# Optimization experiments

Hardware: AMD Instinct MI355X
Metric: run time of the kernel (lower is better)

## Reference

```python
import jax, jax.numpy as jnp
import numpy as np

EPS = 1e-06


def setup_inputs() -> dict:
    key = jax.random.key(0)
    ks = jax.random.split(key, 6)
    B, L, N = 64, 4096, 128
    F = L // 2 + 1  # 2049 rfft bins
    E = 8
    x = jax.random.normal(ks[0], (B, L, N), dtype=jnp.float32)
    band_boundaries = jax.random.normal(ks[1], (E - 1,), dtype=jnp.float32)
    # gate: Linear(F,F) -> ReLU -> Linear(F,E); stored as [in,out] matrices
    gate_w1 = jax.random.normal(ks[2], (F, F), dtype=jnp.float32) * (1.0 / np.sqrt(F))
    gate_b1 = jnp.zeros((F,), dtype=jnp.float32)
    gate_w2 = jax.random.normal(ks[3], (F, E), dtype=jnp.float32) * (1.0 / np.sqrt(F))
    gate_b2 = jnp.zeros((E,), dtype=jnp.float32)
    return {"x": x, "band_boundaries": band_boundaries,
            "gate_w1": gate_w1, "gate_b1": gate_b1,
            "gate_w2": gate_w2, "gate_b2": gate_b2}


def reference(x, band_boundaries, gate_w1, gate_b1, gate_w2, gate_b2):
    # FrequencyMoE forward (residual_add=True). x: [B, L, N]
    B, L, N = x.shape
    F = L // 2 + 1
    xN = jnp.transpose(x, (0, 2, 1))  # [B, N, L]
    mean = jnp.mean(xN, axis=-1, keepdims=True)
    var = jnp.var(xN, axis=-1, keepdims=True) + EPS
    # NOTE: original code computes x_norm then overwrites with xN (normalization skipped),
    # but still rescales the reconstruction by sqrt(var) and adds mean back. Faithful copy.
    freq = jnp.fft.rfft(xN, n=L, axis=-1)  # [B, N, F] complex64

    # learnable band boundaries -> integer bin indices (non-differentiable, as in torch .long())
    bb = jnp.sort(jax.nn.sigmoid(band_boundaries))
    b01 = jnp.concatenate([jnp.zeros((1,), bb.dtype), bb, jnp.ones((1,), bb.dtype)])
    idx = jnp.clip((b01 * F).astype(jnp.int32), 0, F)
    idx = idx.at[-1].set(F)  # [E+1]

    bins = jnp.arange(F)
    # per-expert frequency masks [E, F]: bin in [idx[e], idx[e+1])
    masks = ((bins[None, :] >= idx[:-1, None]) & (bins[None, :] < idx[1:, None])).astype(xN.dtype)

    # gating on mean magnitude spectrum over variables
    mag = jnp.mean(jnp.abs(freq), axis=1)  # [B, F]
    h = jax.nn.relu(mag @ gate_w1 + gate_b1)
    weights = jax.nn.softmax(h @ gate_w2 + gate_b2, axis=-1)  # [B, E]

    # fused weighted-mask combination: sum_e w[b,e]*mask[e,f] applied to spectrum
    wmask = weights @ masks  # [B, F]
    freq_out = freq * wmask[:, None, :]
    x_rec = jnp.fft.irfft(freq_out, n=L, axis=-1)  # [B, N, L]
    x_rec = x_rec * jnp.sqrt(var) + mean
    outN = xN + x_rec  # residual_add=True
    return jnp.transpose(outN, (0, 2, 1))  # [B, L, N]
```

## Files before the change

kernel.cpp:

```cpp
#include <hip/hip_runtime.h>

#define B_ 64
#define L_ 4096
#define N_ 128
#define F_ 2049
#define M_ 2048

__device__ __forceinline__ int pidx(int a) { return a + (a >> 3); }

__device__ __forceinline__ float2 cadd(float2 a, float2 b) { return make_float2(a.x + b.x, a.y + b.y); }
__device__ __forceinline__ float2 csub(float2 a, float2 b) { return make_float2(a.x - b.x, a.y - b.y); }
__device__ __forceinline__ float2 cmul(float2 a, float2 b) {
  return make_float2(a.x * b.x - a.y * b.y, a.x * b.y + a.y * b.x);
}
template <int SGN>
__device__ __forceinline__ float2 mulsi(float2 a) {
  return (SGN > 0) ? make_float2(-a.y, a.x) : make_float2(a.y, -a.x);
}

template <int SGN>
__device__ __forceinline__ void dft8(float2* v) {
  const float C = 0.70710678118654752f;
  float2 t0 = cadd(v[0], v[4]), t1 = csub(v[0], v[4]);
  float2 t2 = cadd(v[2], v[6]), t3 = mulsi<SGN>(csub(v[2], v[6]));
  float2 t4 = cadd(v[1], v[5]), t5 = csub(v[1], v[5]);
  float2 t6 = cadd(v[3], v[7]), t7 = mulsi<SGN>(csub(v[3], v[7]));
  float2 u0 = cadd(t0, t2), u1 = csub(t0, t2);
  float2 u2 = cadd(t1, t3), u3 = csub(t1, t3);
  float2 u4 = cadd(t4, t6), u5 = csub(t4, t6);
  float2 u6 = cadd(t5, t7), u7 = csub(t5, t7);
  float2 w1 = make_float2(C, (SGN > 0) ? C : -C);
  float2 w3 = make_float2(-C, (SGN > 0) ? C : -C);
  float2 a5 = mulsi<SGN>(u5);
  float2 b6 = cmul(u6, w1);
  float2 b7 = cmul(u7, w3);
  v[0] = cadd(u0, u4); v[4] = csub(u0, u4);
  v[2] = cadd(u1, a5); v[6] = csub(u1, a5);
  v[1] = cadd(u2, b6); v[5] = csub(u2, b6);
  v[3] = cadd(u3, b7); v[7] = csub(u3, b7);
}

template <int SGN>
__device__ __forceinline__ void dft4(float2* v) {
  float2 e0 = cadd(v[0], v[2]), e1 = csub(v[0], v[2]);
  float2 o0 = cadd(v[1], v[3]), o1 = mulsi<SGN>(csub(v[1], v[3]));
  v[0] = cadd(e0, o0); v[2] = csub(e0, o0);
  v[1] = cadd(e1, o1); v[3] = csub(e1, o1);
}

template <int SGN>
__device__ __forceinline__ void tw8(float2* v, int pm) {
  float ang = (float)pm * 0.00306796157577128245f;
  float sv, cv;
  __sincosf(ang, &sv, &cv);
  float2 w = make_float2(cv, (SGN > 0) ? sv : -sv);
  float2 wk = w;
  v[1] = cmul(v[1], wk);
#pragma unroll
  for (int k = 2; k < 8; ++k) { wk = cmul(wk, w); v[k] = cmul(v[k], wk); }
}

template <int SGN>
__device__ __forceinline__ void fft2048(float2* __restrict__ buf, float2* v, int t) {
  dft8<SGN>(v);
  tw8<SGN>(v, t);
  __syncthreads();
#pragma unroll
  for (int k = 0; k < 8; ++k) buf[pidx(8 * t + k)] = v[k];
  __syncthreads();
#pragma unroll
  for (int r = 0; r < 8; ++r) v[r] = buf[pidx(t + 256 * r)];
  dft8<SGN>(v);
  tw8<SGN>(v, t & ~7);
  __syncthreads();
  {
    int q = t & 7, p = t >> 3;
#pragma unroll
    for (int k = 0; k < 8; ++k) buf[pidx(q + 8 * (8 * p + k))] = v[k];
  }
  __syncthreads();
#pragma unroll
  for (int r = 0; r < 8; ++r) v[r] = buf[pidx(t + 256 * r)];
  dft8<SGN>(v);
  tw8<SGN>(v, t & ~63);
  __syncthreads();
  {
    int q = t & 63, p = t >> 6;
#pragma unroll
    for (int k = 0; k < 8; ++k) buf[pidx(q + 64 * (8 * p + k))] = v[k];
  }
  __syncthreads();
  float2 w0[4], w1s[4];
#pragma unroll
  for (int r = 0; r < 4; ++r) {
    w0[r] = buf[pidx(t + 512 * r)];
    w1s[r] = buf[pidx(t + 256 + 512 * r)];
  }
  dft4<SGN>(w0);
  dft4<SGN>(w1s);
  __syncthreads();
#pragma unroll
  for (int k = 0; k < 4; ++k) {
    buf[pidx(t + 512 * k)] = w0[k];
    buf[pidx(t + 256 + 512 * k)] = w1s[k];
  }
  __syncthreads();
}

__global__ __launch_bounds__(256) void transpose_k(const float* __restrict__ in,
                                                   float* __restrict__ out,
                                                   int R, int C) {
  __shared__ float tile[32][33];
  const float* ip = in + (size_t)blockIdx.z * R * C;
  float* op = out + (size_t)blockIdx.z * R * C;
  int c0 = blockIdx.x * 32;
  int r0 = blockIdx.y * 32;
  int x = threadIdx.x;
  int y = threadIdx.y;
#pragma unroll
  for (int i = 0; i < 4; ++i)
    tile[y + 8 * i][x] = ip[(size_t)(r0 + y + 8 * i) * C + (c0 + x)];
  __syncthreads();
#pragma unroll
  for (int i = 0; i < 4; ++i)
    op[(size_t)(c0 + y + 8 * i) * R + (r0 + x)] = tile[x][y + 8 * i];
}

template <int S>
__global__ __launch_bounds__(256) void p1_fft_mag(const float* __restrict__ src,
                                                  float* __restrict__ magsum) {
  __shared__ float2 buf[2304];
  int t = threadIdx.x;
  int blk = blockIdx.x;
  int b = blk >> 7;
  int n = blk & 127;
  const float* base = (S == 1) ? (src + (size_t)blk * L_)
                               : (src + (size_t)b * L_ * N_ + n);
  float2 v[8];
  if (S == 1) {
    const float2* r2 = (const float2*)base;
#pragma unroll
    for (int r = 0; r < 8; ++r) v[r] = r2[t + 256 * r];
  } else {
#pragma unroll
    for (int r = 0; r < 8; ++r) {
      int k = t + 256 * r;
      v[r] = make_float2(base[(size_t)(2 * k) * S], base[(size_t)(2 * k + 1) * S]);
    }
  }
  fft2048<-1>(buf, v, t);

  float* msum = magsum + (size_t)b * F_;
#pragma unroll
  for (int i = 0; i < 8; ++i) {
    int f = t + 256 * i;
    float mg;
    if (f == 0) {
      float2 z = buf[pidx(0)];
      mg = fabsf(z.x + z.y);
      atomicAdd(&msum[2048], fabsf(z.x - z.y));
    } else {
      float2 zf = buf[pidx(f)], zm = buf[pidx(2048 - f)];
      float Are = 0.5f * (zf.x + zm.x), Aim = 0.5f * (zf.y - zm.y);
      float Bre = 0.5f * (zf.y + zm.y), Bim = -0.5f * (zf.x - zm.x);
      float ang = (float)f * 0.00153398078788564117f;
      float sv, cv;
      __sincosf(ang, &sv, &cv);
      float Xre = Are + cv * Bre + sv * Bim;
      float Xim = Aim + cv * Bim - sv * Bre;
      mg = sqrtf(Xre * Xre + Xim * Xim);
    }
    atomicAdd(&msum[f], mg);
  }
}

__global__ __launch_bounds__(128) void g1_gemm(const float* __restrict__ mag,
                                               const float* __restrict__ W1,
                                               float* __restrict__ hsum) {
  __shared__ float mt[64][72];
  int o = blockIdx.x * 128 + threadIdx.x;
  int i0 = blockIdx.y * 129;
  int i1 = min(F_, i0 + 129);
  float acc[64];
#pragma unroll
  for (int b = 0; b < 64; ++b) acc[b] = 0.f;
  for (int ic = i0; ic < i1; ic += 64) {
    int nn = min(64, i1 - ic);
    for (int idx = threadIdx.x; idx < 64 * 64; idx += 128) {
      int bb = idx >> 6, ii = idx & 63;
      mt[ii][bb] = (ii < nn) ? mag[bb * F_ + ic + ii] * (1.0f / 128.0f) : 0.f;
    }
    __syncthreads();
    if (o < F_) {
      for (int ii = 0; ii < nn; ++ii) {
        float w = W1[(size_t)(ic + ii) * F_ + o];
        const float4* m4 = (const float4*)&mt[ii][0];
#pragma unroll
        for (int b4 = 0; b4 < 16; ++b4) {
          float4 m = m4[b4];
          acc[4 * b4 + 0] += m.x * w;
          acc[4 * b4 + 1] += m.y * w;
          acc[4 * b4 + 2] += m.z * w;
          acc[4 * b4 + 3] += m.w * w;
        }
      }
    }
    __syncthreads();
  }
  if (o < F_) {
#pragma unroll
    for (int b = 0; b < 64; ++b) atomicAdd(&hsum[(size_t)b * F_ + o], acc[b]);
  }
}

__global__ __launch_bounds__(256) void g2_gate(const float* __restrict__ hsum,
                                               const float* __restrict__ gb1,
                                               const float* __restrict__ W2,
                                               const float* __restrict__ gb2,
                                               const float* __restrict__ bbs,
                                               float* __restrict__ wmask) {
  __shared__ float red[256 * 8];
  __shared__ float wsm[8];
  __shared__ int idxs[9];
  int b = blockIdx.x;
  int t = threadIdx.x;
  float p[8];
#pragma unroll
  for (int e = 0; e < 8; ++e) p[e] = 0.f;
  for (int o = t; o < F_; o += 256) {
    float hv = hsum[(size_t)b * F_ + o] + gb1[o];
    hv = fmaxf(hv, 0.f);
    const float4* w2p = (const float4*)(W2 + (size_t)o * 8);
    float4 wa = w2p[0], wb = w2p[1];
    p[0] += hv * wa.x; p[1] += hv * wa.y; p[2] += hv * wa.z; p[3] += hv * wa.w;
    p[4] += hv * wb.x; p[5] += hv * wb.y; p[6] += hv * wb.z; p[7] += hv * wb.w;
  }
#pragma unroll
  for (int e = 0; e < 8; ++e) red[t * 8 + e] = p[e];
  __syncthreads();
  for (int s = 128; s >= 1; s >>= 1) {
    if (t < s) {
#pragma unroll
      for (int e = 0; e < 8; ++e) red[t * 8 + e] += red[(t + s) * 8 + e];
    }
    __syncthreads();
  }
  if (t == 0) {
    float lg[8];
    float mx = -1e30f;
#pragma unroll
    for (int e = 0; e < 8; ++e) { lg[e] = red[e] + gb2[e]; mx = fmaxf(mx, lg[e]); }
    float sm = 0.f;
#pragma unroll
    for (int e = 0; e < 8; ++e) { lg[e] = expf(lg[e] - mx); sm += lg[e]; }
    float inv = 1.f / sm;
#pragma unroll
    for (int e = 0; e < 8; ++e) wsm[e] = lg[e] * inv;
    float bv[7];
#pragma unroll
    for (int k = 0; k < 7; ++k) bv[k] = 1.f / (1.f + expf(-bbs[k]));
    for (int a = 1; a < 7; ++a) {
      float v = bv[a];
      int j = a - 1;
      while (j >= 0 && bv[j] > v) { bv[j + 1] = bv[j]; --j; }
      bv[j + 1] = v;
    }
    idxs[0] = 0;
    idxs[8] = F_;
    for (int k = 0; k < 7; ++k) {
      int v = (int)(bv[k] * (float)F_);
      v = min(max(v, 0), F_);
      idxs[k + 1] = v;
    }
  }
  __syncthreads();
  for (int f = t; f < F_; f += 256) {
    float wv = 0.f;
#pragma unroll
    for (int e = 0; e < 8; ++e)
      if (f >= idxs[e] && f < idxs[e + 1]) wv = wsm[e];
    wmask[(size_t)b * F_ + f] = wv;
  }
}

template <int S>
__global__ __launch_bounds__(256) void p3_filter(const float* __restrict__ src,
                                                 const float* __restrict__ wmask,
                                                 float* __restrict__ dstp) {
  __shared__ float2 buf[2304];
  __shared__ float sstat[2];
  int t = threadIdx.x;
  int blk = blockIdx.x;
  int b = blk >> 7;
  int n = blk & 127;
  const float* base = (S == 1) ? (src + (size_t)blk * L_)
                               : (src + (size_t)b * L_ * N_ + n);
  float* obase = (S == 1) ? (dstp + (size_t)blk * L_)
                          : (dstp + (size_t)b * L_ * N_ + n);
  float2 v[8];
  float lsum = 0.f, lsq = 0.f;
  if (S == 1) {
    const float2* r2 = (const float2*)base;
#pragma unroll
    for (int r = 0; r < 8; ++r) {
      float2 z = r2[t + 256 * r];
      v[r] = z;
      lsum += z.x + z.y;
      lsq += z.x * z.x + z.y * z.y;
    }
  } else {
#pragma unroll
    for (int r = 0; r < 8; ++r) {
      int k = t + 256 * r;
      float2 z = make_float2(base[(size_t)(2 * k) * S], base[(size_t)(2 * k + 1) * S]);
      v[r] = z;
      lsum += z.x + z.y;
      lsq += z.x * z.x + z.y * z.y;
    }
  }
  for (int off = 32; off > 0; off >>= 1) {
    lsum += __shfl_down(lsum, off);
    lsq += __shfl_down(lsq, off);
  }
  {
    float* rb = (float*)buf;
    int lane = t & 63, wid = t >> 6;
    if (lane == 0) { rb[wid] = lsum; rb[8 + wid] = lsq; }
    __syncthreads();
    if (t == 0) {
      float s1 = rb[0] + rb[1] + rb[2] + rb[3];
      float s2 = rb[8] + rb[9] + rb[10] + rb[11];
      float mean = s1 * (1.0f / 4096.0f);
      float var = s2 * (1.0f / 4096.0f) - mean * mean + 1e-6f;
      sstat[0] = mean;
      sstat[1] = sqrtf(var);
    }
  }
  fft2048<-1>(buf, v, t);

  float mean = sstat[0], sdv = sstat[1];
  const float* wm = wmask + (size_t)b * F_;

  float2 zf_[4], zm_[4];
#pragma unroll
  for (int i = 0; i < 4; ++i) {
    int f = t + 256 * i;
    int fm = (f == 0) ? 1024 : (2048 - f);
    zf_[i] = buf[pidx(f)];
    zm_[i] = buf[pidx(fm)];
  }
  __syncthreads();
#pragma unroll
  for (int i = 0; i < 4; ++i) {
    int f = t + 256 * i;
    if (f == 0) {
      float2 z0 = zf_[0];
      float2 zc = zm_[0];
      float X0 = (z0.x + z0.y) * (1.f + sdv * wm[0]);
      float XM = (z0.x - z0.y) * (1.f + sdv * wm[2048]);
      buf[pidx(0)] = make_float2(0.5f * (X0 + XM), 0.5f * (X0 - XM));
      float mc = 1.f + sdv * wm[1024];
      buf[pidx(1024)] = make_float2(zc.x * mc, zc.y * mc);
    } else {
      float2 zf = zf_[i], zm = zm_[i];
      float Are = 0.5f * (zf.x + zm.x), Aim = 0.5f * (zf.y - zm.y);
      float Bre = 0.5f * (zf.y + zm.y), Bim = -0.5f * (zf.x - zm.x);
      float ang = (float)f * 0.00153398078788564117f;
      float sv, cv;
      __sincosf(ang, &sv, &cv);
      float WBre = cv * Bre + sv * Bim;
      float WBim = cv * Bim - sv * Bre;
      float Xre = Are + WBre, Xim = Aim + WBim;
      float Xmre = Are - WBre, Xmim = -(Aim - WBim);
      float mf = 1.f + sdv * wm[f];
      float mg = 1.f + sdv * wm[2048 - f];
      Xre *= mf; Xim *= mf;
      Xmre *= mg; Xmim *= mg;
      float Apre = 0.5f * (Xre + Xmre), Apim = 0.5f * (Xim - Xmim);
      float Tre = 0.5f * (Xre - Xmre), Tim = 0.5f * (Xim + Xmim);
      float Bpre = cv * Tre - sv * Tim;
      float Bpim = cv * Tim + sv * Tre;
      buf[pidx(f)] = make_float2(Apre - Bpim, Apim + Bpre);
      float Agre = 0.5f * (Xmre + Xre), Agim = 0.5f * (Xmim - Xim);
      float Tgre = 0.5f * (Xmre - Xre), Tgim = 0.5f * (Xmim + Xim);
      float Bgre = -(cv * Tgre + sv * Tgim);
      float Bgim = -(cv * Tgim - sv * Tgre);
      buf[pidx(2048 - f)] = make_float2(Agre - Bgim, Agim + Bgre);
    }
  }
  __syncthreads();
#pragma unroll
  for (int r = 0; r < 8; ++r) v[r] = buf[pidx(t + 256 * r)];
  fft2048<1>(buf, v, t);

  const float inv = 1.0f / 2048.0f;
  if (S == 1) {
    float2* o2 = (float2*)obase;
#pragma unroll
    for (int r = 0; r < 8; ++r) {
      int k = t + 256 * r;
      float2 z = buf[pidx(k)];
      o2[k] = make_float2(z.x * inv + mean, z.y * inv + mean);
    }
  } else {
#pragma unroll
    for (int r = 0; r < 8; ++r) {
      int k = t + 256 * r;
      float2 z = buf[pidx(k)];
      obase[(size_t)(2 * k) * S] = z.x * inv + mean;
      obase[(size_t)(2 * k + 1) * S] = z.y * inv + mean;
    }
  }
}

extern "C" void kernel_launch(void* const* d_in, const int* in_sizes, int n_in,
                              void* d_out, int out_size, void* d_ws,
                              size_t ws_size, hipStream_t stream) {
  const float* x = (const float*)d_in[0];
  const float* bbs = (const float*)d_in[1];
  const float* W1 = (const float*)d_in[2];
  const float* gb1 = (const float*)d_in[3];
  const float* W2 = (const float*)d_in[4];
  const float* gb2 = (const float*)d_in[5];
  float* out = (float*)d_out;

  const size_t bigElems = (size_t)B_ * N_ * L_;
  const size_t smallBytes = (size_t)3 * B_ * F_ * sizeof(float);
  const bool fast = ws_size >= bigElems * sizeof(float) + smallBytes;

  char* smallBase = (char*)d_ws + (fast ? bigElems * sizeof(float) : 0);
  float* magsum = (float*)smallBase;
  float* hsum = magsum + (size_t)B_ * F_;
  float* wmaskp = hsum + (size_t)B_ * F_;
  float* outT = (float*)d_ws;

  hipMemsetAsync(magsum, 0, (size_t)2 * B_ * F_ * sizeof(float), stream);

  dim3 tb(32, 8);
  if (fast) {
    transpose_k<<<dim3(N_ / 32, L_ / 32, B_), tb, 0, stream>>>(x, out, L_, N_);
    p1_fft_mag<1><<<dim3(B_ * N_), 256, 0, stream>>>(out, magsum);
  } else {
    p1_fft_mag<N_><<<dim3(B_ * N_), 256, 0, stream>>>(x, magsum);
  }
  g1_gemm<<<dim3(17, 16), 128, 0, stream>>>(magsum, W1, hsum);
  g2_gate<<<dim3(B_), 256, 0, stream>>>(hsum, gb1, W2, gb2, bbs, wmaskp);
  if (fast) {
    p3_filter<1><<<dim3(B_ * N_), 256, 0, stream>>>(out, wmaskp, outT);
    transpose_k<<<dim3(L_ / 32, N_ / 32, B_), tb, 0, stream>>>(outT, out, N_, L_);
  } else {
    p3_filter<N_><<<dim3(B_ * N_), 256, 0, stream>>>(x, wmaskp, out);
  }
}
```

Baseline: 553.3 us.

## Cache forward FFT spectrum to skip recomputing it in filter pass

```diff
diff --git a/kernel.cpp b/kernel.cpp
--- a/kernel.cpp
+++ b/kernel.cpp
@@ -174,43 +174,73 @@
   }
 }
 
-__global__ __launch_bounds__(128) void g1_gemm(const float* __restrict__ mag,
+__global__ __launch_bounds__(256) void p1_fft_mag_z(const float* __restrict__ src,
+                                                    float2* __restrict__ zout,
+                                                    float* __restrict__ magsum) {
+  __shared__ float2 buf[2304];
+  int t = threadIdx.x;
+  int blk = blockIdx.x;
+  int b = blk >> 7;
+  const float2* r2 = (const float2*)(src + (size_t)blk * L_);
+  float2 v[8];
+#pragma unroll
+  for (int r = 0; r < 8; ++r) v[r] = r2[t + 256 * r];
+  fft2048<-1>(buf, v, t);
+
+  float* msum = magsum + (size_t)b * F_;
+  float2* zrow = zout + (size_t)blk * (size_t)M_;
+#pragma unroll
+  for (int i = 0; i < 8; ++i) {
+    int f = t + 256 * i;
+    float mg;
+    if (f == 0) {
+      float2 z = buf[pidx(0)];
+      zrow[0] = z;
+      mg = fabsf(z.x + z.y);
+      atomicAdd(&msum[2048], fabsf(z.x - z.y));
+    } else {
+      float2 zf = buf[pidx(f)], zm = buf[pidx(2048 - f)];
+      zrow[f] = zf;
+      float Are = 0.5f * (zf.x + zm.x), Aim = 0.5f * (zf.y - zm.y);
+      float Bre = 0.5f * (zf.y + zm.y), Bim = -0.5f * (zf.x - zm.x);
+      float ang = (float)f * 0.00153398078788564117f;
+      float sv, cv;
+      __sincosf(ang, &sv, &cv);
+      float Xre = Are + cv * Bre + sv * Bim;
+      float Xim = Aim + cv * Bim - sv * Bre;
+      mg = sqrtf(Xre * Xre + Xim * Xim);
+    }
+    atomicAdd(&msum[f], mg);
+  }
+}
+
+__global__ __launch_bounds__(256) void magt_k(const float* __restrict__ mag,
+                                              float* __restrict__ magT) {
+  int idx = blockIdx.x * 256 + threadIdx.x;
+  if (idx >= 64 * F_) return;
+  int f = idx >> 6, b = idx & 63;
+  magT[idx] = mag[(size_t)b * F_ + f] * (1.0f / 128.0f);
+}
+
+#define G1K 33
+__global__ __launch_bounds__(256) void g1_gemm(const float* __restrict__ magT,
                                                const float* __restrict__ W1,
                                                float* __restrict__ hsum) {
-  __shared__ float mt[64][72];
-  int o = blockIdx.x * 128 + threadIdx.x;
-  int i0 = blockIdx.y * 129;
-  int i1 = min(F_, i0 + 129);
+  int o = blockIdx.x * 256 + threadIdx.x;
+  if (o >= F_) return;
+  int i0 = blockIdx.y * G1K;
+  int i1 = min(F_, i0 + G1K);
   float acc[64];
 #pragma unroll
   for (int b = 0; b < 64; ++b) acc[b] = 0.f;
-  for (int ic = i0; ic < i1; ic += 64) {
-    int nn = min(64, i1 - ic);
-    for (int idx = threadIdx.x; idx < 64 * 64; idx += 128) {
-      int bb = idx >> 6, ii = idx & 63;
-      mt[ii][bb] = (ii < nn) ? mag[bb * F_ + ic + ii] * (1.0f / 128.0f) : 0.f;
-    }
-    __syncthreads();
-    if (o < F_) {
-      for (int ii = 0; ii < nn; ++ii) {
-        float w = W1[(size_t)(ic + ii) * F_ + o];
-        const float4* m4 = (const float4*)&mt[ii][0];
-#pragma unroll
-        for (int b4 = 0; b4 < 16; ++b4) {
-          float4 m = m4[b4];
-          acc[4 * b4 + 0] += m.x * w;
-          acc[4 * b4 + 1] += m.y * w;
-          acc[4 * b4 + 2] += m.z * w;
-          acc[4 * b4 + 3] += m.w * w;
-        }
-      }
-    }
-    __syncthreads();
-  }
-  if (o < F_) {
-#pragma unroll
-    for (int b = 0; b < 64; ++b) atomicAdd(&hsum[(size_t)b * F_ + o], acc[b]);
-  }
+  for (int i = i0; i < i1; ++i) {
+    float w = W1[(size_t)i * F_ + o];
+    const float* mrow = magT + (size_t)i * 64;
+#pragma unroll
+    for (int b = 0; b < 64; ++b) acc[b] = fmaf(mrow[b], w, acc[b]);
+  }
+#pragma unroll
+  for (int b = 0; b < 64; ++b) atomicAdd(&hsum[(size_t)b * F_ + o], acc[b]);
 }
 
 __global__ __launch_bounds__(256) void g2_gate(const float* __restrict__ hsum,
@@ -283,60 +313,41 @@
   }
 }
 
-template <int S>
-__global__ __launch_bounds__(256) void p3_filter(const float* __restrict__ src,
-                                                 const float* __restrict__ wmask,
-                                                 float* __restrict__ dstp) {
+__global__ __launch_bounds__(256) void p3_filter_z(float2* __restrict__ zbuf,
+                                                   const float* __restrict__ wmask) {
   __shared__ float2 buf[2304];
+  __shared__ float rb[8];
   __shared__ float sstat[2];
   int t = threadIdx.x;
   int blk = blockIdx.x;
   int b = blk >> 7;
-  int n = blk & 127;
-  const float* base = (S == 1) ? (src + (size_t)blk * L_)
-                               : (src + (size_t)b * L_ * N_ + n);
-  float* obase = (S == 1) ? (dstp + (size_t)blk * L_)
-                          : (dstp + (size_t)b * L_ * N_ + n);
+  float2* zrow = zbuf + (size_t)blk * (size_t)M_;
   float2 v[8];
-  float lsum = 0.f, lsq = 0.f;
-  if (S == 1) {
-    const float2* r2 = (const float2*)base;
-#pragma unroll
-    for (int r = 0; r < 8; ++r) {
-      float2 z = r2[t + 256 * r];
-      v[r] = z;
-      lsum += z.x + z.y;
-      lsq += z.x * z.x + z.y * z.y;
-    }
-  } else {
-#pragma unroll
-    for (int r = 0; r < 8; ++r) {
-      int k = t + 256 * r;
-      float2 z = make_float2(base[(size_t)(2 * k) * S], base[(size_t)(2 * k + 1) * S]);
-      v[r] = z;
-      lsum += z.x + z.y;
-      lsq += z.x * z.x + z.y * z.y;
-    }
-  }
-  for (int off = 32; off > 0; off >>= 1) {
-    lsum += __shfl_down(lsum, off);
-    lsq += __shfl_down(lsq, off);
-  }
+  float lsq = 0.f;
+#pragma unroll
+  for (int r = 0; r < 8; ++r) {
+    float2 z = zrow[t + 256 * r];
+    v[r] = z;
+    lsq += z.x * z.x + z.y * z.y;
+  }
+#pragma unroll
+  for (int r = 0; r < 8; ++r) buf[pidx(t + 256 * r)] = v[r];
+  for (int off = 32; off > 0; off >>= 1) lsq += __shfl_down(lsq, off);
   {
-    float* rb = (float*)buf;
     int lane = t & 63, wid = t >> 6;
-    if (lane == 0) { rb[wid] = lsum; rb[8 + wid] = lsq; }
-    __syncthreads();
-    if (t == 0) {
-      float s1 = rb[0] + rb[1] + rb[2] + rb[3];
-      float s2 = rb[8] + rb[9] + rb[10] + rb[11];
-      float mean = s1 * (1.0f / 4096.0f);
-      float var = s2 * (1.0f / 4096.0f) - mean * mean + 1e-6f;
-      sstat[0] = mean;
-      sstat[1] = sqrtf(var);
-    }
-  }
-  fft2048<-1>(buf, v, t);
+    if (lane == 0) rb[wid] = lsq;
+  }
+  __syncthreads();
+  if (t == 0) {
+    float s2 = rb[0] + rb[1] + rb[2] + rb[3];
+    float2 z0 = buf[pidx(0)];
+    float mean = (z0.x + z0.y) * (1.0f / 4096.0f);
+    float sumsq = s2 * (1.0f / 2048.0f);
+    float var = sumsq * (1.0f / 4096.0f) - mean * mean + 1e-6f;
+    sstat[0] = mean;
+    sstat[1] = sqrtf(var);
+  }
+  __syncthreads();
 
   float mean = sstat[0], sdv = sstat[1];
   const float* wm = wmask + (size_t)b * F_;
@@ -394,6 +405,125 @@
   fft2048<1>(buf, v, t);
 
   const float inv = 1.0f / 2048.0f;
+#pragma unroll
+  for (int r = 0; r < 8; ++r) {
+    int k = t + 256 * r;
+    float2 z = buf[pidx(k)];
+    zrow[k] = make_float2(z.x * inv + mean, z.y * inv + mean);
+  }
+}
+
+template <int S>
+__global__ __launch_bounds__(256) void p3_filter(const float* __restrict__ src,
+                                                 const float* __restrict__ wmask,
+                                                 float* __restrict__ dstp) {
+  __shared__ float2 buf[2304];
+  __shared__ float sstat[2];
+  int t = threadIdx.x;
+  int blk = blockIdx.x;
+  int b = blk >> 7;
+  int n = blk & 127;
+  const float* base = (S == 1) ? (src + (size_t)blk * L_)
+                               : (src + (size_t)b * L_ * N_ + n);
+  float* obase = (S == 1) ? (dstp + (size_t)blk * L_)
+                          : (dstp + (size_t)b * L_ * N_ + n);
+  float2 v[8];
+  float lsum = 0.f, lsq = 0.f;
+  if (S == 1) {
+    const float2* r2 = (const float2*)base;
+#pragma unroll
+    for (int r = 0; r < 8; ++r) {
+      float2 z = r2[t + 256 * r];
+      v[r] = z;
+      lsum += z.x + z.y;
+      lsq += z.x * z.x + z.y * z.y;
+    }
+  } else {
+#pragma unroll
+    for (int r = 0; r < 8; ++r) {
+      int k = t + 256 * r;
+      float2 z = make_float2(base[(size_t)(2 * k) * S], base[(size_t)(2 * k + 1) * S]);
+      v[r] = z;
+      lsum += z.x + z.y;
+      lsq += z.x * z.x + z.y * z.y;
+    }
+  }
+  for (int off = 32; off > 0; off >>= 1) {
+    lsum += __shfl_down(lsum, off);
+    lsq += __shfl_down(lsq, off);
+  }
+  {
+    float* rb = (float*)buf;
+    int lane = t & 63, wid = t >> 6;
+    if (lane == 0) { rb[wid] = lsum; rb[8 + wid] = lsq; }
+    __syncthreads();
+    if (t == 0) {
+      float s1 = rb[0] + rb[1] + rb[2] + rb[3];
+      float s2 = rb[8] + rb[9] + rb[10] + rb[11];
+      float mean = s1 * (1.0f / 4096.0f);
+      float var = s2 * (1.0f / 4096.0f) - mean * mean + 1e-6f;
+      sstat[0] = mean;
+      sstat[1] = sqrtf(var);
+    }
+  }
+  fft2048<-1>(buf, v, t);
+
+  float mean = sstat[0], sdv = sstat[1];
+  const float* wm = wmask + (size_t)b * F_;
+
+  float2 zf_[4], zm_[4];
+#pragma unroll
+  for (int i = 0; i < 4; ++i) {
+    int f = t + 256 * i;
+    int fm = (f == 0) ? 1024 : (2048 - f);
+    zf_[i] = buf[pidx(f)];
+    zm_[i] = buf[pidx(fm)];
+  }
+  __syncthreads();
+#pragma unroll
+  for (int i = 0; i < 4; ++i) {
+    int f = t + 256 * i;
+    if (f == 0) {
+      float2 z0 = zf_[0];
+      float2 zc = zm_[0];
+      float X0 = (z0.x + z0.y) * (1.f + sdv * wm[0]);
+      float XM = (z0.x - z0.y) * (1.f + sdv * wm[2048]);
+      buf[pidx(0)] = make_float2(0.5f * (X0 + XM), 0.5f * (X0 - XM));
+      float mc = 1.f + sdv * wm[1024];
+      buf[pidx(1024)] = make_float2(zc.x * mc, zc.y * mc);
+    } else {
+      float2 zf = zf_[i], zm = zm_[i];
+      float Are = 0.5f * (zf.x + zm.x), Aim = 0.5f * (zf.y - zm.y);
+      float Bre = 0.5f * (zf.y + zm.y), Bim = -0.5f * (zf.x - zm.x);
+      float ang = (float)f * 0.00153398078788564117f;
+      float sv, cv;
+      __sincosf(ang, &sv, &cv);
+      float WBre = cv * Bre + sv * Bim;
+      float WBim = cv * Bim - sv * Bre;
+      float Xre = Are + WBre, Xim = Aim + WBim;
+      float Xmre = Are - WBre, Xmim = -(Aim - WBim);
+      float mf = 1.f + sdv * wm[f];
+      float mg = 1.f + sdv * wm[2048 - f];
+      Xre *= mf; Xim *= mf;
+      Xmre *= mg; Xmim *= mg;
+      float Apre = 0.5f * (Xre + Xmre), Apim = 0.5f * (Xim - Xmim);
+      float Tre = 0.5f * (Xre - Xmre), Tim = 0.5f * (Xim + Xmim);
+      float Bpre = cv * Tre - sv * Tim;
+      float Bpim = cv * Tim + sv * Tre;
+      buf[pidx(f)] = make_float2(Apre - Bpim, Apim + Bpre);
+      float Agre = 0.5f * (Xmre + Xre), Agim = 0.5f * (Xmim - Xim);
+      float Tgre = 0.5f * (Xmre - Xre), Tgim = 0.5f * (Xmim + Xim);
+      float Bgre = -(cv * Tgre + sv * Tgim);
+      float Bgim = -(cv * Tgim - sv * Tgre);
+      buf[pidx(2048 - f)] = make_float2(Agre - Bgim, Agim + Bgre);
+    }
+  }
+  __syncthreads();
+#pragma unroll
+  for (int r = 0; r < 8; ++r) v[r] = buf[pidx(t + 256 * r)];
+  fft2048<1>(buf, v, t);
+
+  const float inv = 1.0f / 2048.0f;
   if (S == 1) {
     float2* o2 = (float2*)obase;
 #pragma unroll
@@ -432,23 +562,27 @@
   float* magsum = (float*)smallBase;
   float* hsum = magsum + (size_t)B_ * F_;
   float* wmaskp = hsum + (size_t)B_ * F_;
-  float* outT = (float*)d_ws;
 
   hipMemsetAsync(magsum, 0, (size_t)2 * B_ * F_ * sizeof(float), stream);
 
   dim3 tb(32, 8);
+  const int g1x = (F_ + 255) / 256;
+  const int g1y = (F_ + G1K - 1) / G1K;
+  const int mtb = (64 * F_ + 255) / 256;
   if (fast) {
+    float2* Z = (float2*)d_ws;
     transpose_k<<<dim3(N_ / 32, L_ / 32, B_), tb, 0, stream>>>(x, out, L_, N_);
-    p1_fft_mag<1><<<dim3(B_ * N_), 256, 0, stream>>>(out, magsum);
+    p1_fft_mag_z<<<dim3(B_ * N_), 256, 0, stream>>>(out, Z, magsum);
+    magt_k<<<dim3(mtb), 256, 0, stream>>>(magsum, wmaskp);
+    g1_gemm<<<dim3(g1x, g1y), 256, 0, stream>>>(wmaskp, W1, hsum);
+    g2_gate<<<dim3(B_), 256, 0, stream>>>(hsum, gb1, W2, gb2, bbs, wmaskp);
+    p3_filter_z<<<dim3(B_ * N_), 256, 0, stream>>>(Z, wmaskp);
+    transpose_k<<<dim3(L_ / 32, N_ / 32, B_), tb, 0, stream>>>((float*)d_ws, out, N_, L_);
   } else {
     p1_fft_mag<N_><<<dim3(B_ * N_), 256, 0, stream>>>(x, magsum);
-  }
-  g1_gemm<<<dim3(17, 16), 128, 0, stream>>>(magsum, W1, hsum);
-  g2_gate<<<dim3(B_), 256, 0, stream>>>(hsum, gb1, W2, gb2, bbs, wmaskp);
-  if (fast) {
-    p3_filter<1><<<dim3(B_ * N_), 256, 0, stream>>>(out, wmaskp, outT);
-    transpose_k<<<dim3(L_ / 32, N_ / 32, B_), tb, 0, stream>>>(outT, out, N_, L_);
-  } else {
+    magt_k<<<dim3(mtb), 256, 0, stream>>>(magsum, wmaskp);
+    g1_gemm<<<dim3(g1x, g1y), 256, 0, stream>>>(wmaskp, W1, hsum);
+    g2_gate<<<dim3(B_), 256, 0, stream>>>(hsum, gb1, W2, gb2, bbs, wmaskp);
     p3_filter<N_><<<dim3(B_ * N_), 256, 0, stream>>>(x, wmaskp, out);
   }
 }
```

After: 492.0 us. 1.12x faster.
